# Kernel optimization log

Hardware: AMD Instinct MI355X
Metric: run time of the kernel (lower is better)

The kernel has to match this reference:

```python
import jax, jax.numpy as jnp
import numpy as np
from jax import lax

SR, N_FFT, HOP, N_MELS = 32000, 2048, 512, 128
F_MIN, F_MAX = 20.0, 16000.0
EPS, S, ALPHA, DELTA, R = 1e-6, 0.025, 0.98, 2.0, 0.5


def _hz_to_mel(f):
    return 2595.0 * np.log10(1.0 + np.asarray(f, np.float64) / 700.0)


def _mel_to_hz(m):
    return 700.0 * (10.0 ** (np.asarray(m, np.float64) / 2595.0) - 1.0)


def _mel_filterbank():
    # torchaudio melscale_fbanks, mel_scale='htk', norm=None -> [n_freqs, n_mels]
    n_freqs = N_FFT // 2 + 1
    all_freqs = np.linspace(0.0, SR / 2.0, n_freqs)
    m_pts = np.linspace(_hz_to_mel(F_MIN), _hz_to_mel(F_MAX), N_MELS + 2)
    f_pts = _mel_to_hz(m_pts)                      # [n_mels+2]
    f_diff = np.diff(f_pts)                        # [n_mels+1]
    slopes = f_pts[None, :] - all_freqs[:, None]   # [n_freqs, n_mels+2]
    down = -slopes[:, :-2] / f_diff[:-1]
    up = slopes[:, 2:] / f_diff[1:]
    fb = np.maximum(0.0, np.minimum(down, up))
    return jnp.asarray(fb, jnp.float32)            # [1025, 128]


def _hann_window():
    # periodic Hann window (torch.hann_window default)
    n = np.arange(N_FFT)
    return jnp.asarray(0.5 - 0.5 * np.cos(2.0 * np.pi * n / N_FFT), jnp.float32)


def setup_inputs() -> dict:
    key = jax.random.key(0)
    waveform = jax.random.normal(key, (64, 160000), dtype=jnp.float32)
    return {"waveform": waveform}


def _pcen(mel_bmt):
    # mel_bmt: [B, M, T]; IIR smoother m_t = (1-s) m_{t-1} + s x_t
    x_tbm = jnp.transpose(mel_bmt, (2, 0, 1))  # [T, B, M]
    m0 = jnp.zeros(x_tbm.shape[1:], x_tbm.dtype)

    def step(m, xt):
        m = (1.0 - S) * m + S * xt
        p = (xt / (EPS + m) ** ALPHA + DELTA) ** R - DELTA ** R
        return m, p

    _, out = lax.scan(step, m0, x_tbm)
    return jnp.transpose(out, (1, 2, 0))  # [B, M, T]


def reference(waveform) -> jnp.ndarray:
    if waveform.ndim == 1:
        waveform = waveform[None, :]
    pad = N_FFT // 2
    x = jnp.pad(waveform, ((0, 0), (pad, pad)), mode="reflect")
    n_frames = 1 + waveform.shape[1] // HOP  # 313
    idx = np.arange(n_frames)[:, None] * HOP + np.arange(N_FFT)[None, :]
    frames = x[:, idx] * _hann_window()                    # [B, T, n_fft]
    spec = jnp.fft.rfft(frames, axis=-1)                   # [B, T, 1025]
    power = spec.real ** 2 + spec.imag ** 2                # power=2.0
    mel = jnp.einsum("btf,fm->bmt", power, _mel_filterbank())  # [B, 128, T]
    mel = _pcen(mel)
    return mel[:, None, :, :]  # [B, 1, 128, 313]
```

## Files before the change

kernel.cpp:

```cpp
#include <hip/hip_runtime.h>

#define PI_D 3.14159265358979323846

#define BATCH   64
#define LWAV    160000
#define NFFT    2048
#define HOP     512
#define NMELS   128
#define NFRAMES 313
#define NCPLX   1024
#define PADW    1024

#define NCH     16
#define CHLEN   20

#define OFF_WIN  0
#define OFF_LEN  2048
#define OFF_KK   2176
#define OFF_WW   10496
#define OFF_MFIN 18816
#define OFF_MEL  149888

#define LROW 17
#define TSTR (64 * LROW)
#define SW4(u) ((((u)&3)<<2)|((u)>>2))
#define CMULC(xr, xi, cr, ci) { float _t = (xr); (xr) = _t*(cr) - (xi)*(ci); (xi) = _t*(ci) + (xi)*(cr); }
#define WVB() { __builtin_amdgcn_wave_barrier(); asm volatile("" ::: "memory"); }

__device__ __forceinline__ double melpt(int i) {
    double mlo = 2595.0 * log10(1.0 + 20.0 / 700.0);
    double mhi = 2595.0 * log10(1.0 + 16000.0 / 700.0);
    double m = mlo + (mhi - mlo) * (double)i / 129.0;
    return 700.0 * (pow(10.0, m / 2595.0) - 1.0);
}

__global__ __launch_bounds__(256) void init_tables(float* __restrict__ ws) {
    const int tid = threadIdx.x;
    const int blk = blockIdx.x;
    if (blk < 8) {
        int i = blk * 256 + tid;
        double w = 0.5 - 0.5 * cos(2.0 * PI_D * (double)i / (double)NFFT);
        ws[OFF_WIN + i] = (float)w;
        return;
    }
    if (tid >= NMELS) return;
    const int m = tid;
    double fp0 = melpt(m), fp1 = melpt(m + 1), fp2 = melpt(m + 2);
    int* kk = (int*)(ws + OFF_KK);
    float* wwt = ws + OFF_WW;
    int k0 = (int)(fp0 / 15.625); if (k0 < 1) k0 = 1;
    int k1 = (int)(fp2 / 15.625) + 1; if (k1 > 1023) k1 = 1023;
    int cnt = 0;
    for (int k = k0; k <= k1; k++) {
        double f = (double)k * 15.625;
        double down = (f - fp0) / (fp1 - fp0);
        double up   = (fp2 - f) / (fp2 - fp1);
        double w = down < up ? down : up;
        if (w > 0.0 && cnt < 64) {
            kk[cnt * NMELS + m] = k;
            wwt[cnt * NMELS + m] = (float)w;
            cnt++;
        }
    }
    ((int*)(ws + OFF_LEN))[m] = cnt;
    for (int e = cnt; e < 65; e++) {
        kk[e * NMELS + m] = 0;
        wwt[e * NMELS + m] = 0.f;
    }
}

__device__ __forceinline__ void fft4s(float* yr, float* yi, int i0, int i1, int i2, int i3) {
    float t0r = yr[i0] + yr[i2], t0i = yi[i0] + yi[i2];
    float t1r = yr[i0] - yr[i2], t1i = yi[i0] - yi[i2];
    float t2r = yr[i1] + yr[i3], t2i = yi[i1] + yi[i3];
    float t3r = yr[i1] - yr[i3], t3i = yi[i1] - yi[i3];
    yr[i0] = t0r + t2r; yi[i0] = t0i + t2i;
    yr[i1] = t1r + t3i; yi[i1] = t1i - t3r;
    yr[i2] = t0r - t2r; yi[i2] = t0i - t2i;
    yr[i3] = t1r - t3i; yi[i3] = t1i + t3r;
}

__device__ __forceinline__ void fft16(float* yr, float* yi) {
    fft4s(yr, yi, 0, 4, 8, 12);
    fft4s(yr, yi, 1, 5, 9, 13);
    fft4s(yr, yi, 2, 6, 10, 14);
    fft4s(yr, yi, 3, 7, 11, 15);
    CMULC(yr[5],  yi[5],   0.92387953f, -0.38268343f);
    CMULC(yr[9],  yi[9],   0.70710678f, -0.70710678f);
    CMULC(yr[13], yi[13],  0.38268343f, -0.92387953f);
    CMULC(yr[6],  yi[6],   0.70710678f, -0.70710678f);
    { float _t = yr[10]; yr[10] = yi[10]; yi[10] = -_t; }
    CMULC(yr[14], yi[14], -0.70710678f, -0.70710678f);
    CMULC(yr[7],  yi[7],   0.38268343f, -0.92387953f);
    CMULC(yr[11], yi[11], -0.70710678f, -0.70710678f);
    CMULC(yr[15], yi[15], -0.92387953f,  0.38268343f);
    fft4s(yr, yi, 0, 1, 2, 3);
    fft4s(yr, yi, 4, 5, 6, 7);
    fft4s(yr, yi, 8, 9, 10, 11);
    fft4s(yr, yi, 12, 13, 14, 15);
}

__global__ __launch_bounds__(256) void fft_mel_kernel(const float* __restrict__ wav,
                                                      float* __restrict__ ws) {
    __shared__ float T[4][TSTR];
    const int tid  = threadIdx.x;
    const int wv   = tid >> 6;
    const int lane = tid & 63;
    const int frame = blockIdx.x * 4 + wv;
    const int b = frame / NFRAMES;
    const int t = frame - b * NFRAMES;

    float yr[16], yi[16];
    const float* __restrict__ src = wav + (size_t)b * LWAV;
    const int base = t * HOP - PADW;
    const float2* __restrict__ win2 = (const float2*)(ws + OFF_WIN);

    if (base >= 0 && base + NFFT <= LWAV) {
        const float2* __restrict__ s2 = (const float2*)(src + base);
#pragma unroll
        for (int c = 0; c < 16; c++) {
            int n = lane + 64 * c;
            float2 xv = s2[n];
            float2 wq = win2[n];
            yr[c] = xv.x * wq.x;
            yi[c] = xv.y * wq.y;
        }
    } else {
#pragma unroll
        for (int c = 0; c < 16; c++) {
            int n = lane + 64 * c;
            int i0 = base + 2 * n, i1 = i0 + 1;
            i0 = i0 < 0 ? -i0 : i0; i0 = i0 >= LWAV ? 2 * LWAV - 2 - i0 : i0;
            i1 = i1 < 0 ? -i1 : i1; i1 = i1 >= LWAV ? 2 * LWAV - 2 - i1 : i1;
            float2 wq = win2[n];
            yr[c] = src[i0] * wq.x;
            yi[c] = src[i1] * wq.y;
        }
    }

    fft16(yr, yi);

    {
        float wr_, wi_;
        __sincosf(-6.13592315e-3f * (float)lane, &wi_, &wr_);
        float cr = wr_, ci = wi_;
#pragma unroll
        for (int u = 1; u < 16; u++) {
            CMULC(yr[SW4(u)], yi[SW4(u)], cr, ci);
            if (u < 15) { CMULC(cr, ci, wr_, wi_); }
        }
    }

    float* __restrict__ tb = T[wv];
    const int a = lane & 15, g = lane >> 4;
    const int wbase = lane * LROW;
    const int rbase = a * LROW + 4 * g;
    {
#pragma unroll
        for (int u = 0; u < 16; u++) tb[wbase + u] = yr[SW4(u)];
        WVB();
#pragma unroll
        for (int bq = 0; bq < 4; bq++)
#pragma unroll
            for (int m = 0; m < 4; m++)
                yr[4 * bq + m] = tb[rbase + bq * (16 * LROW) + m];
        WVB();
#pragma unroll
        for (int u = 0; u < 16; u++) tb[wbase + u] = yi[SW4(u)];
        WVB();
#pragma unroll
        for (int bq = 0; bq < 4; bq++)
#pragma unroll
            for (int m = 0; m < 4; m++)
                yi[4 * bq + m] = tb[rbase + bq * (16 * LROW) + m];
        WVB();
    }

#pragma unroll
    for (int m = 0; m < 4; m++) fft4s(yr, yi, m, 4 + m, 8 + m, 12 + m);

    {
        float w1r, w1i;
        __sincosf(-9.81747704e-2f * (float)a, &w1i, &w1r);
        float w2r = w1r * w1r - w1i * w1i, w2i = 2.f * w1r * w1i;
        float w3r = w1r * w2r - w1i * w2i, w3i = w1r * w2i + w1i * w2r;
#pragma unroll
        for (int m = 0; m < 4; m++) {
            CMULC(yr[4 + m],  yi[4 + m],  w1r, w1i);
            CMULC(yr[8 + m],  yi[8 + m],  w2r, w2i);
            CMULC(yr[12 + m], yi[12 + m], w3r, w3i);
        }
    }

    {
        const int a2 = 68 * g + a;
        const int rb2 = lane * LROW;
#pragma unroll
        for (int s = 0; s < 4; s++)
#pragma unroll
            for (int m = 0; m < 4; m++)
                tb[a2 + LROW * (16 * s + m)] = yr[4 * s + m];
        WVB();
#pragma unroll
        for (int aa = 0; aa < 16; aa++) yr[aa] = tb[rb2 + aa];
        WVB();
#pragma unroll
        for (int s = 0; s < 4; s++)
#pragma unroll
            for (int m = 0; m < 4; m++)
                tb[a2 + LROW * (16 * s + m)] = yi[4 * s + m];
        WVB();
#pragma unroll
        for (int aa = 0; aa < 16; aa++) yi[aa] = tb[rb2 + aa];
        WVB();
    }

    fft16(yr, yi);

    {
        const int pl = (64 - lane) & 63;
        float er, ei;
        __sincosf(-3.06796158e-3f * (float)lane, &ei, &er);
        float prevR = __shfl(yr[0], pl, 64), prevI = __shfl(yi[0], pl, 64);
#pragma unroll
        for (int tt = 0; tt < 16; tt++) {
            const int sl = SW4(15 - tt);
            float curR = __shfl(yr[sl], pl, 64), curI = __shfl(yi[sl], pl, 64);
            float pr = (lane == 0) ? prevR : curR;
            float pi = (lane == 0) ? prevI : curI;
            const int ms = SW4(tt);
            float zr = yr[ms], zi = yi[ms];
            float Ar = 0.5f * (zr + pr), Ai = 0.5f * (zi - pi);
            float Or = 0.5f * (zi + pi), Oi = -0.5f * (zr - pr);
            float Xr = Ar + er * Or - ei * Oi;
            float Xi = Ai + er * Oi + ei * Or;
            tb[lane + 64 * tt] = Xr * Xr + Xi * Xi;
            prevR = curR; prevI = curI;
            CMULC(er, ei, 0.98078528f, -0.19509032f);
        }
    }
    __syncthreads();

    {
        const int m = tid & 127;
        const int h = tid >> 7;
        const int L = ((const int*)(ws + OFF_LEN))[m];
        const int* __restrict__ kk = (const int*)(ws + OFF_KK);
        const float* __restrict__ wwt = ws + OFF_WW;
        const float* __restrict__ P0 = T[2 * h];
        const float* __restrict__ P1 = T[2 * h + 1];
        float a0 = 0.f, a1 = 0.f;
        int k = kk[m];
        float w = wwt[m];
        for (int e = 0; e < L; e++) {
            int k2 = kk[(e + 1) * NMELS + m];
            float w2 = wwt[(e + 1) * NMELS + m];
            a0 = fmaf(w, P0[k], a0);
            a1 = fmaf(w, P1[k], a1);
            k = k2; w = w2;
        }
        const int fr0 = blockIdx.x * 4 + 2 * h;
        const int b0 = fr0 / NFRAMES, t0 = fr0 - b0 * NFRAMES;
        const int fr1 = fr0 + 1;
        const int b1 = fr1 / NFRAMES, t1 = fr1 - b1 * NFRAMES;
        ws[OFF_MEL + (size_t)t0 * (BATCH * NMELS) + b0 * NMELS + m] = a0;
        ws[OFF_MEL + (size_t)t1 * (BATCH * NMELS) + b1 * NMELS + m] = a1;
    }
}

__global__ __launch_bounds__(128) void pcen_scan1(float* __restrict__ ws) {
    const int bx = blockIdx.x;
    const int b = bx >> 4, c = bx & 15;
    const int tid = threadIdx.x;
    const int t0 = c * CHLEN;
    const int len = (c == NCH - 1) ? (NFRAMES - t0) : CHLEN;
    const float* __restrict__ mel = ws + OFF_MEL + b * NMELS + tid;
    float m = 0.f;
#pragma unroll 5
    for (int t = 0; t < len; t++) {
        float x = mel[(size_t)(t0 + t) * (BATCH * NMELS)];
        m = fmaf(0.975f, m, 0.025f * x);
    }
    ws[OFF_MFIN + (b * NCH + c) * NMELS + tid] = m;
}

__global__ __launch_bounds__(128) void pcen_scan2(const float* __restrict__ ws,
                                                  float* __restrict__ out) {
    __shared__ float tile[CHLEN * 129];
    const int bx = blockIdx.x;
    const int b = bx >> 4, c = bx & 15;
    const int tid = threadIdx.x;
    const int t0 = c * CHLEN;
    const int len = (c == NCH - 1) ? (NFRAMES - t0) : CHLEN;
    double Apd = 1.0;
    for (int i = 0; i < CHLEN; i++) Apd *= 0.975;
    const float Ap = (float)Apd;
    float m = 0.f;
    const float* __restrict__ mfin = ws + OFF_MFIN + b * NCH * NMELS + tid;
    for (int cc = 0; cc < c; cc++) m = fmaf(Ap, m, mfin[cc * NMELS]);
    const float* __restrict__ mel = ws + OFF_MEL + b * NMELS + tid;
    for (int t = 0; t < len; t++) {
        float x = mel[(size_t)(t0 + t) * (BATCH * NMELS)];
        m = fmaf(0.975f, m, 0.025f * x);
        float d = 1e-6f + m;
        float pd = exp2f(-0.98f * __log2f(d));
        float p = sqrtf(fmaf(x, pd, 2.0f)) - 1.41421356237f;
        tile[t * 129 + tid] = p;
    }
    __syncthreads();
    for (int idx = tid; idx < len * 128; idx += 128) {
        int row = idx / len, col = idx - row * len;
        out[(size_t)(b * NMELS + row) * NFRAMES + t0 + col] = tile[col * 129 + row];
    }
}

extern "C" void kernel_launch(void* const* d_in, const int* in_sizes, int n_in,
                              void* d_out, int out_size, void* d_ws, size_t ws_size,
                              hipStream_t stream) {
    const float* wav = (const float*)d_in[0];
    float* out = (float*)d_out;
    float* ws = (float*)d_ws;
    init_tables<<<9, 256, 0, stream>>>(ws);
    fft_mel_kernel<<<(BATCH * NFRAMES) / 4, 256, 0, stream>>>(wav, ws);
    pcen_scan1<<<BATCH * NCH, 128, 0, stream>>>(ws);
    pcen_scan2<<<BATCH * NCH, 128, 0, stream>>>(ws, out);
}
```

Measured before the change: 155.5 us.

## Use XOR-swizzled float4 LDS transposes and rebalance mel projection across waves

Replaces the padded (stride-17) scalar LDS transposes in the FFT with XOR-swizzled float4 stores and loads, which cuts the number of LDS instructions while aiming to stay free of bank conflicts. The mel filterbank step now has each thread pair handle one mel bin for all four frames, splitting the filter taps between the two lanes and combining them with a shuffle, so each weight and index load is reused four times. The PCEN output loop gets constant divisors for the full and tail chunks so the compiler can drop the runtime integer division. Risks are extra register pressure from the wider vectors and divergent loop lengths within a wave in the mel loop.

```diff
diff --git a/kernel.cpp b/kernel.cpp
--- a/kernel.cpp
+++ b/kernel.cpp
@@ -21,8 +21,6 @@
 #define OFF_MFIN 18816
 #define OFF_MEL  149888
 
-#define LROW 17
-#define TSTR (64 * LROW)
 #define SW4(u) ((((u)&3)<<2)|((u)>>2))
 #define CMULC(xr, xi, cr, ci) { float _t = (xr); (xr) = _t*(cr) - (xi)*(ci); (xi) = _t*(ci) + (xi)*(cr); }
 #define WVB() { __builtin_amdgcn_wave_barrier(); asm volatile("" ::: "memory"); }
@@ -102,7 +100,7 @@
 
 __global__ __launch_bounds__(256) void fft_mel_kernel(const float* __restrict__ wav,
                                                       float* __restrict__ ws) {
-    __shared__ float T[4][TSTR];
+    __shared__ float T[4][1024];
     const int tid  = threadIdx.x;
     const int wv   = tid >> 6;
     const int lane = tid & 63;
@@ -152,27 +150,34 @@
     }
 
     float* __restrict__ tb = T[wv];
+    float4* __restrict__ tb4 = (float4*)tb;
     const int a = lane & 15, g = lane >> 4;
-    const int wbase = lane * LROW;
-    const int rbase = a * LROW + 4 * g;
-    {
-#pragma unroll
-        for (int u = 0; u < 16; u++) tb[wbase + u] = yr[SW4(u)];
-        WVB();
-#pragma unroll
-        for (int bq = 0; bq < 4; bq++)
-#pragma unroll
-            for (int m = 0; m < 4; m++)
-                yr[4 * bq + m] = tb[rbase + bq * (16 * LROW) + m];
-        WVB();
-#pragma unroll
-        for (int u = 0; u < 16; u++) tb[wbase + u] = yi[SW4(u)];
-        WVB();
-#pragma unroll
-        for (int bq = 0; bq < 4; bq++)
-#pragma unroll
-            for (int m = 0; m < 4; m++)
-                yi[4 * bq + m] = tb[rbase + bq * (16 * LROW) + m];
+    {
+#pragma unroll
+        for (int c = 0; c < 4; c++) {
+            float4 v; v.x = yr[c]; v.y = yr[4 + c]; v.z = yr[8 + c]; v.w = yr[12 + c];
+            tb4[lane * 4 + (c ^ (lane & 3))] = v;
+        }
+        WVB();
+#pragma unroll
+        for (int bq = 0; bq < 4; bq++) {
+            int r = a + 16 * bq;
+            float4 v = tb4[r * 4 + (g ^ (r & 3))];
+            yr[4 * bq] = v.x; yr[4 * bq + 1] = v.y; yr[4 * bq + 2] = v.z; yr[4 * bq + 3] = v.w;
+        }
+        WVB();
+#pragma unroll
+        for (int c = 0; c < 4; c++) {
+            float4 v; v.x = yi[c]; v.y = yi[4 + c]; v.z = yi[8 + c]; v.w = yi[12 + c];
+            tb4[lane * 4 + (c ^ (lane & 3))] = v;
+        }
+        WVB();
+#pragma unroll
+        for (int bq = 0; bq < 4; bq++) {
+            int r = a + 16 * bq;
+            float4 v = tb4[r * 4 + (g ^ (r & 3))];
+            yi[4 * bq] = v.x; yi[4 * bq + 1] = v.y; yi[4 * bq + 2] = v.z; yi[4 * bq + 3] = v.w;
+        }
         WVB();
     }
 
@@ -193,25 +198,25 @@
     }
 
     {
-        const int a2 = 68 * g + a;
-        const int rb2 = lane * LROW;
-#pragma unroll
-        for (int s = 0; s < 4; s++)
-#pragma unroll
-            for (int m = 0; m < 4; m++)
-                tb[a2 + LROW * (16 * s + m)] = yr[4 * s + m];
-        WVB();
-#pragma unroll
-        for (int aa = 0; aa < 16; aa++) yr[aa] = tb[rb2 + aa];
-        WVB();
-#pragma unroll
-        for (int s = 0; s < 4; s++)
-#pragma unroll
-            for (int m = 0; m < 4; m++)
-                tb[a2 + LROW * (16 * s + m)] = yi[4 * s + m];
-        WVB();
-#pragma unroll
-        for (int aa = 0; aa < 16; aa++) yi[aa] = tb[rb2 + aa];
+#pragma unroll
+        for (int s = 0; s < 4; s++) {
+            float4 v; v.x = yr[4 * s]; v.y = yr[4 * s + 1]; v.z = yr[4 * s + 2]; v.w = yr[4 * s + 3];
+            tb4[a * 16 + ((4 * s + g) ^ a)] = v;
+        }
+        WVB();
+#pragma unroll
+        for (int aa = 0; aa < 16; aa++)
+            yr[aa] = tb[aa * 64 + 4 * ((lane >> 2) ^ aa) + (lane & 3)];
+        WVB();
+#pragma unroll
+        for (int s = 0; s < 4; s++) {
+            float4 v; v.x = yi[4 * s]; v.y = yi[4 * s + 1]; v.z = yi[4 * s + 2]; v.w = yi[4 * s + 3];
+            tb4[a * 16 + ((4 * s + g) ^ a)] = v;
+        }
+        WVB();
+#pragma unroll
+        for (int aa = 0; aa < 16; aa++)
+            yi[aa] = tb[aa * 64 + 4 * ((lane >> 2) ^ aa) + (lane & 3)];
         WVB();
     }
 
@@ -242,29 +247,37 @@
     __syncthreads();
 
     {
-        const int m = tid & 127;
-        const int h = tid >> 7;
+        const int m = 32 * wv + (lane >> 1);
+        const int p = lane & 1;
         const int L = ((const int*)(ws + OFF_LEN))[m];
         const int* __restrict__ kk = (const int*)(ws + OFF_KK);
         const float* __restrict__ wwt = ws + OFF_WW;
-        const float* __restrict__ P0 = T[2 * h];
-        const float* __restrict__ P1 = T[2 * h + 1];
-        float a0 = 0.f, a1 = 0.f;
-        int k = kk[m];
-        float w = wwt[m];
-        for (int e = 0; e < L; e++) {
-            int k2 = kk[(e + 1) * NMELS + m];
-            float w2 = wwt[(e + 1) * NMELS + m];
+        const float* __restrict__ P0 = T[0];
+        const float* __restrict__ P1 = T[1];
+        const float* __restrict__ P2 = T[2];
+        const float* __restrict__ P3 = T[3];
+        float a0 = 0.f, a1 = 0.f, a2 = 0.f, a3 = 0.f;
+        for (int e = p; e < L; e += 2) {
+            int k = kk[e * NMELS + m];
+            float w = wwt[e * NMELS + m];
             a0 = fmaf(w, P0[k], a0);
             a1 = fmaf(w, P1[k], a1);
-            k = k2; w = w2;
-        }
-        const int fr0 = blockIdx.x * 4 + 2 * h;
-        const int b0 = fr0 / NFRAMES, t0 = fr0 - b0 * NFRAMES;
-        const int fr1 = fr0 + 1;
-        const int b1 = fr1 / NFRAMES, t1 = fr1 - b1 * NFRAMES;
-        ws[OFF_MEL + (size_t)t0 * (BATCH * NMELS) + b0 * NMELS + m] = a0;
-        ws[OFF_MEL + (size_t)t1 * (BATCH * NMELS) + b1 * NMELS + m] = a1;
+            a2 = fmaf(w, P2[k], a2);
+            a3 = fmaf(w, P3[k], a3);
+        }
+        a0 += __shfl_xor(a0, 1, 64);
+        a1 += __shfl_xor(a1, 1, 64);
+        a2 += __shfl_xor(a2, 1, 64);
+        a3 += __shfl_xor(a3, 1, 64);
+        if (p == 0) {
+            float acc[4] = {a0, a1, a2, a3};
+#pragma unroll
+            for (int f = 0; f < 4; f++) {
+                const int fr = blockIdx.x * 4 + f;
+                const int bb = fr / NFRAMES, tt = fr - bb * NFRAMES;
+                ws[OFF_MEL + (size_t)tt * (BATCH * NMELS) + bb * NMELS + m] = acc[f];
+            }
+        }
     }
 }
 
@@ -308,9 +321,16 @@
         tile[t * 129 + tid] = p;
     }
     __syncthreads();
-    for (int idx = tid; idx < len * 128; idx += 128) {
-        int row = idx / len, col = idx - row * len;
-        out[(size_t)(b * NMELS + row) * NFRAMES + t0 + col] = tile[col * 129 + row];
+    if (len == CHLEN) {
+        for (int idx = tid; idx < CHLEN * 128; idx += 128) {
+            int row = idx / CHLEN, col = idx - row * CHLEN;
+            out[(size_t)(b * NMELS + row) * NFRAMES + t0 + col] = tile[col * 129 + row];
+        }
+    } else {
+        for (int idx = tid; idx < 13 * 128; idx += 128) {
+            int row = idx / 13, col = idx - row * 13;
+            out[(size_t)(b * NMELS + row) * NFRAMES + t0 + col] = tile[col * 129 + row];
+        }
     }
 }
 
```

After: 162.2 us. +4.3%, slower.
